# Kernel optimization log

Hardware: AMD Instinct MI355X
Metric: run time of the kernel (lower is better)

Reference implementation:

```python
import jax, jax.numpy as jnp
import numpy as np

HIDDEN = 1024
N_HEADS = 16
HEAD_DIM = HIDDEN // N_HEADS  # 64
SCALE = HEAD_DIM ** -0.5
B, QL, KVL = 2, 2048, 4096


def setup_inputs() -> dict:
    key = jax.random.key(0)
    ks = jax.random.split(key, 7)
    s = 0.02
    return {
        "query_states": jax.random.normal(ks[0], (B, QL, HIDDEN), jnp.float32),
        "key_states": jax.random.normal(ks[1], (B, KVL, HIDDEN), jnp.float32),
        "value_states": jax.random.normal(ks[2], (B, KVL, HIDDEN), jnp.float32),
        # torch nn.Linear weights: shape [out, in], applied as x @ W.T
        "Wq": jax.random.normal(ks[3], (HIDDEN, HIDDEN), jnp.float32) * s,
        "Wk": jax.random.normal(ks[4], (HIDDEN, HIDDEN), jnp.float32) * s,
        "Wv": jax.random.normal(ks[5], (HIDDEN, HIDDEN), jnp.float32) * s,
        "Wo": jax.random.normal(ks[6], (HIDDEN, HIDDEN), jnp.float32) * s,
    }


def reference(query_states, key_states, value_states, Wq, Wk, Wv, Wo):
    b, ql, _ = query_states.shape
    kvl = key_states.shape[1]
    # projections (torch Linear: x @ W.T)
    q = query_states @ Wq.T  # [b, ql, H]
    k = key_states @ Wk.T    # [b, kvl, H]
    v = value_states @ Wv.T  # [b, kvl, H]
    # split heads -> [b, h, s, d]
    q = q.reshape(b, ql, N_HEADS, HEAD_DIM).transpose(0, 2, 1, 3)
    k = k.reshape(b, kvl, N_HEADS, HEAD_DIM).transpose(0, 2, 1, 3)
    v = v.reshape(b, kvl, N_HEADS, HEAD_DIM).transpose(0, 2, 1, 3)
    # scores [b, h, ql, kvl]
    scores = jnp.einsum("bhqd,bhkd->bhqk", q, k) * SCALE
    attn = jax.nn.softmax(scores, axis=-1)
    out = jnp.einsum("bhqk,bhkd->bhqd", attn, v)  # [b, h, ql, d]
    out = out.transpose(0, 2, 1, 3).reshape(b, ql, HIDDEN)
    return out @ Wo.T
```

## Files before the change

### kernel.cpp

```cpp
#include <hip/hip_runtime.h>

#define HID   1024
#define NH    16
#define HD    64
#define QL    2048
#define KVL   4096
#define NB    2
#define QSCALE 0.180336880111120426f

typedef short s8v  __attribute__((ext_vector_type(8)));
typedef short s4v  __attribute__((ext_vector_type(4)));
typedef float f4v  __attribute__((ext_vector_type(4)));

__device__ __forceinline__ unsigned short f2bf(float f) {
  unsigned int u = __builtin_bit_cast(unsigned int, f);
  u += 0x7FFFu + ((u >> 16) & 1u);
  return (unsigned short)(u >> 16);
}
__device__ __forceinline__ float bf2f(unsigned short h) {
  unsigned int u = ((unsigned int)h) << 16;
  return __builtin_bit_cast(float, u);
}
__device__ __forceinline__ float fexp2(float x) {
#if __has_builtin(__builtin_amdgcn_exp2f)
  return __builtin_amdgcn_exp2f(x);
#else
  return exp2f(x);
#endif
}

__global__ __launch_bounds__(256)
void cast_all(const float* __restrict__ q, const float* __restrict__ k,
              const float* __restrict__ v, const float* __restrict__ wq,
              const float* __restrict__ wk, const float* __restrict__ wv,
              const float* __restrict__ wo, unsigned short* __restrict__ dst) {
  size_t c = (size_t)blockIdx.x * 256 + threadIdx.x;
  const float* src; size_t lc; float sc = 1.0f;
  if (c < 524288)       { src = q;  lc = c; }
  else if (c < 1572864) { src = k;  lc = c - 524288; }
  else if (c < 2621440) { src = v;  lc = c - 1572864; }
  else if (c < 2752512) { src = wq; lc = c - 2621440; sc = QSCALE; }
  else if (c < 2883584) { src = wk; lc = c - 2752512; }
  else if (c < 3014656) { src = wv; lc = c - 2883584; }
  else                  { src = wo; lc = c - 3014656; }
  const float4* p = (const float4*)(src + lc * 8);
  float4 a = p[0], b = p[1];
  union { s8v v8; unsigned short h[8]; } u;
  u.h[0] = f2bf(a.x * sc); u.h[1] = f2bf(a.y * sc);
  u.h[2] = f2bf(a.z * sc); u.h[3] = f2bf(a.w * sc);
  u.h[4] = f2bf(b.x * sc); u.h[5] = f2bf(b.y * sc);
  u.h[6] = f2bf(b.z * sc); u.h[7] = f2bf(b.w * sc);
  *(s8v*)(dst + c * 8) = u.v8;
}

typedef const __attribute__((address_space(1))) unsigned int* gas_t;
typedef __attribute__((address_space(3))) unsigned int*       las_t;

__device__ __forceinline__ void gl_lds16(const unsigned short* g, unsigned short* l) {
  __builtin_amdgcn_global_load_lds((gas_t)(const void*)g, (las_t)(void*)l, 16, 0, 0);
}

template <bool OUT_BF16>
__device__ __forceinline__ void gemm_body(const unsigned short* __restrict__ A,
                                          const unsigned short* __restrict__ B,
                                          void* __restrict__ Cv, int N, int K,
                                          int bx, int by,
                                          unsigned short (*As)[128 * 32],
                                          unsigned short (*Bs)[128 * 32]) {
  const int tid  = threadIdx.x;
  const int wave = tid >> 6, lane = tid & 63;
  const int wm = wave >> 1, wn = wave & 1;
  const int quad = lane >> 4, l15 = lane & 15;
  const int row0 = by * 128;
  const int col0 = bx * 128;
  const int srow = lane >> 2;
  const int scol = (lane & 3) * 8;

  f4v acc[4][4] = {};

#define G_STAGE(KI, BI)                                                         \
  {                                                                             \
    _Pragma("unroll")                                                           \
    for (int cc = 0; cc < 2; cc++) {                                            \
      int c = wave + cc * 4;                                                    \
      gl_lds16(A + (size_t)(row0 + c * 16 + srow) * K + (KI) * 32 + scol,       \
               &As[BI][c * 512]);                                               \
      gl_lds16(B + (size_t)(col0 + c * 16 + srow) * K + (KI) * 32 + scol,       \
               &Bs[BI][c * 512]);                                               \
    }                                                                           \
  }

  const int nk = K >> 5;
  G_STAGE(0, 0);
  __syncthreads();

  for (int ki = 0; ki < nk; ki++) {
    const int cur = ki & 1;
    if (ki + 1 < nk) G_STAGE(ki + 1, 1 - cur);

    s8v af[4], bf[4];
#pragma unroll
    for (int i = 0; i < 4; i++)
      af[i] = *(const s8v*)&As[cur][(wm * 64 + i * 16 + l15) * 32 + quad * 8];
#pragma unroll
    for (int j = 0; j < 4; j++)
      bf[j] = *(const s8v*)&Bs[cur][(wn * 64 + j * 16 + l15) * 32 + quad * 8];
#pragma unroll
    for (int i = 0; i < 4; i++)
#pragma unroll
      for (int j = 0; j < 4; j++)
        acc[i][j] = __builtin_amdgcn_mfma_f32_16x16x32_bf16(af[i], bf[j],
                                                            acc[i][j], 0, 0, 0);
    __syncthreads();
  }
#undef G_STAGE

#pragma unroll
  for (int i = 0; i < 4; i++) {
#pragma unroll
    for (int j = 0; j < 4; j++) {
      int r = row0 + wm * 64 + i * 16 + quad * 4;
      int c = col0 + wn * 64 + j * 16 + l15;
#pragma unroll
      for (int reg = 0; reg < 4; reg++) {
        float v = acc[i][j][reg];
        if constexpr (OUT_BF16)
          ((unsigned short*)Cv)[(size_t)(r + reg) * N + c] = f2bf(v);
        else
          ((float*)Cv)[(size_t)(r + reg) * N + c] = v;
      }
    }
  }
}

__global__ __launch_bounds__(256, 4)
void proj_fused(const unsigned short* __restrict__ qc, const unsigned short* __restrict__ kc,
                const unsigned short* __restrict__ vc, const unsigned short* __restrict__ wqc,
                const unsigned short* __restrict__ wkc, const unsigned short* __restrict__ wvc,
                unsigned short* __restrict__ qp, unsigned short* __restrict__ kp,
                unsigned short* __restrict__ vpt) {
  __shared__ unsigned short As[2][128 * 32];
  __shared__ unsigned short Bs[2][128 * 32];
  int bid = blockIdx.x;
  if (bid < 256) {
    gemm_body<true>(qc, wqc, qp, HID, HID, bid & 7, bid >> 3, As, Bs);
  } else if (bid < 768) {
    int l = bid - 256;
    gemm_body<true>(kc, wkc, kp, HID, HID, l & 7, l >> 3, As, Bs);
  } else {
    int l = bid - 768;
    int b = l >> 8, r = l & 255;
    gemm_body<true>(wvc, vc + (size_t)b * KVL * HID,
                    vpt + (size_t)b * HID * KVL, KVL, HID, r & 31, r >> 5, As, Bs);
  }
}

__global__ __launch_bounds__(256, 4)
void o_gemm(const unsigned short* __restrict__ ao, const unsigned short* __restrict__ woc,
            float* __restrict__ out) {
  __shared__ unsigned short As[2][128 * 32];
  __shared__ unsigned short Bs[2][128 * 32];
  int bid = blockIdx.x;
  gemm_body<false>(ao, woc, out, HID, HID, bid & 7, bid >> 3, As, Bs);
}

#define LDSK 40

template <typename T>
__device__ __forceinline__ void stage_tile(unsigned short* dst, const T* src,
                                           int ld, int tid, float sc) {
#pragma unroll
  for (int rep = 0; rep < 2; rep++) {
    int s = rep * 256 + tid;
    int row = s >> 2;
    int cs  = (s & 3) * 8;
    const T* p = src + (size_t)row * ld + cs;
    s8v val;
    if constexpr (sizeof(T) == 4) {
      float4 f0 = *(const float4*)p;
      float4 f1 = *(const float4*)(p + 4);
      union { s8v v; unsigned short h[8]; } u;
      u.h[0] = f2bf(f0.x * sc); u.h[1] = f2bf(f0.y * sc);
      u.h[2] = f2bf(f0.z * sc); u.h[3] = f2bf(f0.w * sc);
      u.h[4] = f2bf(f1.x * sc); u.h[5] = f2bf(f1.y * sc);
      u.h[6] = f2bf(f1.z * sc); u.h[7] = f2bf(f1.w * sc);
      val = u.v;
    } else {
      val = *(const s8v*)p;
    }
    *(s8v*)&dst[row * LDSK + cs] = val;
  }
}

template <typename TA, typename TB, bool OUT_BF16>
__global__ __launch_bounds__(256)
void gemm_conv(const TA* __restrict__ A, const TB* __restrict__ B,
               void* __restrict__ Cv, int M, int N, int K, float bscale,
               long long bz, long long cz) {
  __shared__ unsigned short As[128 * LDSK];
  __shared__ unsigned short Bs[128 * LDSK];
  const TB* Bp = B + (size_t)blockIdx.z * (size_t)bz;
  const int tid  = threadIdx.x;
  const int wave = tid >> 6, lane = tid & 63;
  const int wm = wave >> 1, wn = wave & 1;
  const int quad = lane >> 4, l15 = lane & 15;
  const int row0 = blockIdx.y * 128;
  const int col0 = blockIdx.x * 128;

  f4v acc[4][4] = {};

  for (int k0 = 0; k0 < K; k0 += 32) {
    __syncthreads();
    stage_tile(As, A + (size_t)row0 * K + k0, K, tid, 1.0f);
    stage_tile(Bs, Bp + (size_t)col0 * K + k0, K, tid, bscale);
    __syncthreads();

    s8v af[4], bf[4];
#pragma unroll
    for (int i = 0; i < 4; i++)
      af[i] = *(const s8v*)&As[(wm * 64 + i * 16 + l15) * LDSK + quad * 8];
#pragma unroll
    for (int j = 0; j < 4; j++)
      bf[j] = *(const s8v*)&Bs[(wn * 64 + j * 16 + l15) * LDSK + quad * 8];
#pragma unroll
    for (int i = 0; i < 4; i++)
#pragma unroll
      for (int j = 0; j < 4; j++)
        acc[i][j] = __builtin_amdgcn_mfma_f32_16x16x32_bf16(af[i], bf[j],
                                                            acc[i][j], 0, 0, 0);
  }

  char* Cp = (char*)Cv + (size_t)blockIdx.z * (size_t)cz * (OUT_BF16 ? 2 : 4);
#pragma unroll
  for (int i = 0; i < 4; i++) {
#pragma unroll
    for (int j = 0; j < 4; j++) {
      int r = row0 + wm * 64 + i * 16 + quad * 4;
      int c = col0 + wn * 64 + j * 16 + l15;
#pragma unroll
      for (int reg = 0; reg < 4; reg++) {
        float v = acc[i][j][reg];
        if constexpr (OUT_BF16)
          ((unsigned short*)Cp)[(size_t)(r + reg) * N + c] = f2bf(v);
        else
          ((float*)Cp)[(size_t)(r + reg) * N + c] = v;
      }
    }
  }
}

template <bool SPLIT>
__global__ __launch_bounds__(256, 2)
void attn6(const unsigned short* __restrict__ qp,
           const unsigned short* __restrict__ kp,
           const unsigned short* __restrict__ vpt,
           unsigned short* __restrict__ po,
           float* __restrict__ pl,
           unsigned short* __restrict__ ao) {
  __shared__ unsigned short Ks[2][64 * 64];
  __shared__ unsigned short Vt[2][64 * 64];
  __shared__ unsigned short Pt[4][64 * 64];

  const int bid  = blockIdx.x;
  const int qb   = bid & 7;
  const int h    = (bid >> 3) & 15;
  const int b    = (bid >> 7) & 1;
  const int half = SPLIT ? (bid >> 8) : 0;
  const int tid  = threadIdx.x;
  const int wave = tid >> 6, lane = tid & 63;
  const int quad = lane >> 4, l15 = lane & 15;
  const int q0   = qb * 256 + wave * 64;
  const int kvoff = half * (KVL / 2);
  const int NT   = SPLIT ? (KVL / 128) : (KVL / 64);

  const unsigned short* kbase = kp + (size_t)b * KVL * HID + h * HD + (size_t)kvoff * HID;
  const unsigned short* vbase = vpt + (size_t)(b * NH + h) * HD * KVL + kvoff;

  int prow[2], pcol[2], pbase[2];
#pragma unroll
  for (int i = 0; i < 2; i++) {
    int p = (i * 4 + wave) * 64 + lane;
    prow[i]  = p >> 3;
    pcol[i]  = ((p & 7) ^ (prow[i] & 7)) * 8;
    pbase[i] = (i * 4 + wave) * 512;
  }

  s8v qf[4][2];
#pragma unroll
  for (int nt = 0; nt < 4; nt++) {
    const size_t qrow = (size_t)(b * QL + q0 + nt * 16 + l15) * HID + h * HD;
#pragma unroll
    for (int ks = 0; ks < 2; ks++)
      qf[nt][ks] = *(const s8v*)(qp + qrow + ks * 32 + quad * 8);
  }

  float lrun[4] = {0.f, 0.f, 0.f, 0.f};
  f4v oacc[4][4] = {};

#define STAGE_KV(KT, BI)                                                        \
  {                                                                             \
    const unsigned short* kb = kbase + (size_t)((KT) * 64) * HID;               \
    const unsigned short* vb = vbase + (KT) * 64;                               \
    _Pragma("unroll")                                                           \
    for (int i = 0; i < 2; i++) {                                               \
      gl_lds16(kb + (size_t)prow[i] * HID + pcol[i], &Ks[BI][pbase[i]]);        \
      gl_lds16(vb + (size_t)prow[i] * KVL + pcol[i], &Vt[BI][pbase[i]]);        \
    }                                                                           \
  }

  STAGE_KV(0, 0);
  __syncthreads();

  for (int kt = 0; kt < NT; kt++) {
    const int cur = kt & 1;
    if (kt + 1 < NT) STAGE_KV(kt + 1, 1 - cur);

    f4v sacc[4][4] = {};
#pragma unroll
    for (int ks = 0; ks < 2; ks++)
#pragma unroll
      for (int mt = 0; mt < 4; mt++) {
        int row = mt * 16 + l15;
        int xc  = ((ks * 4 + quad) ^ (row & 7)) * 8;
        s8v kf = *(const s8v*)&Ks[cur][row * 64 + xc];
#pragma unroll
        for (int nt = 0; nt < 4; nt++)
          sacc[mt][nt] = __builtin_amdgcn_mfma_f32_16x16x32_bf16(kf, qf[nt][ks],
                                                                 sacc[mt][nt], 0, 0, 0);
      }

#pragma unroll
    for (int nt = 0; nt < 4; nt++) {
      float rs = 0.f;
#pragma unroll
      for (int mt = 0; mt < 4; mt++) {
        float p0 = fexp2(sacc[mt][nt][0]);
        float p1 = fexp2(sacc[mt][nt][1]);
        float p2 = fexp2(sacc[mt][nt][2]);
        float p3 = fexp2(sacc[mt][nt][3]);
        rs += (p0 + p1) + (p2 + p3);
        union { s4v v4; unsigned short hh[4]; } pk;
        pk.hh[0] = (unsigned short)(__builtin_bit_cast(unsigned int, p0) >> 16);
        pk.hh[1] = (unsigned short)(__builtin_bit_cast(unsigned int, p1) >> 16);
        pk.hh[2] = (unsigned short)(__builtin_bit_cast(unsigned int, p2) >> 16);
        pk.hh[3] = (unsigned short)(__builtin_bit_cast(unsigned int, p3) >> 16);
        int row = nt * 16 + l15;
        int c   = mt * 2 + (quad >> 1);
        int off = ((c ^ (row & 7)) * 8) + (quad & 1) * 4;
        *(s4v*)&Pt[wave][row * 64 + off] = pk.v4;
      }
      rs += __shfl_xor(rs, 16, 64);
      rs += __shfl_xor(rs, 32, 64);
      lrun[nt] += rs;
    }

#pragma unroll
    for (int ch = 0; ch < 2; ch++) {
      s8v vf[4];
#pragma unroll
      for (int dt = 0; dt < 4; dt++) {
        int row = dt * 16 + l15;
        int xc  = ((ch * 4 + quad) ^ (row & 7)) * 8;
        vf[dt] = *(const s8v*)&Vt[cur][row * 64 + xc];
      }
#pragma unroll
      for (int qt = 0; qt < 4; qt++) {
        int row = qt * 16 + l15;
        int xc  = ((ch * 4 + quad) ^ (row & 7)) * 8;
        s8v pf = *(const s8v*)&Pt[wave][row * 64 + xc];
#pragma unroll
        for (int dt = 0; dt < 4; dt++)
          oacc[qt][dt] = __builtin_amdgcn_mfma_f32_16x16x32_bf16(pf, vf[dt],
                                                                 oacc[qt][dt], 0, 0, 0);
      }
    }

    __syncthreads();
  }
#undef STAGE_KV

  if constexpr (SPLIT) {
    unsigned short* pob = po + (size_t)half * NB * QL * HID;
#pragma unroll
    for (int qt = 0; qt < 4; qt++) {
#pragma unroll
      for (int dt = 0; dt < 4; dt++)
#pragma unroll
        for (int r = 0; r < 4; r++) {
          int qq = q0 + qt * 16 + quad * 4 + r;
          int cc = h * HD + dt * 16 + l15;
          pob[(size_t)(b * QL + qq) * HID + cc] = f2bf(oacc[qt][dt][r]);
        }
      if (quad == 0)
        pl[(size_t)half * NB * NH * QL + (b * NH + h) * QL + q0 + qt * 16 + l15] = lrun[qt];
    }
  } else {
#pragma unroll
    for (int qt = 0; qt < 4; qt++) {
      float li = 1.0f / lrun[qt];
      float lr[4];
#pragma unroll
      for (int r = 0; r < 4; r++)
        lr[r] = __shfl(li, (lane & 48) + quad * 4 + r, 64);
#pragma unroll
      for (int dt = 0; dt < 4; dt++)
#pragma unroll
        for (int r = 0; r < 4; r++) {
          int qq = q0 + qt * 16 + quad * 4 + r;
          int cc = h * HD + dt * 16 + l15;
          ao[(size_t)(b * QL + qq) * HID + cc] = f2bf(oacc[qt][dt][r] * lr[r]);
        }
    }
  }
}

__global__ __launch_bounds__(256)
void combine(const unsigned short* __restrict__ po, const float* __restrict__ pl,
             unsigned short* __restrict__ ao) {
  int t  = blockIdx.x * 256 + threadIdx.x;
  int r  = t >> 7;
  int c8 = t & 127;
  int b = r >> 11, q = r & 2047, h = c8 >> 3;
  size_t lidx = (size_t)(b * NH + h) * QL + q;
  float l = pl[lidx] + pl[(size_t)NB * NH * QL + lidx];
  float inv = 1.0f / l;
  size_t off = (size_t)r * HID + c8 * 8;
  s8v a = *(const s8v*)(po + off);
  s8v c = *(const s8v*)(po + (size_t)NB * QL * HID + off);
  union { s8v v8; unsigned short hh[8]; } ua, uc, uo;
  ua.v8 = a; uc.v8 = c;
#pragma unroll
  for (int e = 0; e < 8; e++)
    uo.hh[e] = f2bf((bf2f(ua.hh[e]) + bf2f(uc.hh[e])) * inv);
  *(s8v*)(ao + off) = uo.v8;
}

extern "C" void kernel_launch(void* const* d_in, const int* in_sizes, int n_in,
                              void* d_out, int out_size, void* d_ws, size_t ws_size,
                              hipStream_t stream) {
  const float* q  = (const float*)d_in[0];
  const float* k  = (const float*)d_in[1];
  const float* v  = (const float*)d_in[2];
  const float* Wq = (const float*)d_in[3];
  const float* Wk = (const float*)d_in[4];
  const float* Wv = (const float*)d_in[5];
  const float* Wo = (const float*)d_in[6];
  float* out = (float*)d_out;
  char* ws = (char*)d_ws;
  dim3 blk(256);

  const long long MB = 1024 * 1024;
  if (ws_size >= (size_t)88 * MB) {
    unsigned short* qc  = (unsigned short*)(ws);
    unsigned short* kc  = (unsigned short*)(ws + 8 * MB);
    unsigned short* vc  = (unsigned short*)(ws + 24 * MB);
    unsigned short* wqc = (unsigned short*)(ws + 40 * MB);
    unsigned short* wkc = (unsigned short*)(ws + 42 * MB);
    unsigned short* wvc = (unsigned short*)(ws + 44 * MB);
    unsigned short* woc = (unsigned short*)(ws + 46 * MB);
    unsigned short* qp  = (unsigned short*)(ws + 48 * MB);
    unsigned short* kp  = (unsigned short*)(ws + 56 * MB);
    unsigned short* vpt = (unsigned short*)(ws + 72 * MB);
    unsigned short* ao  = (unsigned short*)(ws);
    unsigned short* po  = (unsigned short*)(ws + 8 * MB);
    float*          pl  = (float*)(ws + 40 * MB);

    cast_all<<<12288, blk, 0, stream>>>(q, k, v, Wq, Wk, Wv, Wo, (unsigned short*)ws);
    proj_fused<<<1280, blk, 0, stream>>>(qc, kc, vc, wqc, wkc, wvc, qp, kp, vpt);
    attn6<true><<<512, blk, 0, stream>>>(qp, kp, vpt, po, pl, nullptr);
    combine<<<2048, blk, 0, stream>>>(po, pl, ao);
    o_gemm<<<256, blk, 0, stream>>>(ao, woc, out);
  } else {
    unsigned short* qp  = (unsigned short*)(ws);
    unsigned short* kp  = (unsigned short*)(ws + 8 * MB);
    unsigned short* vpt = (unsigned short*)(ws + 24 * MB);
    unsigned short* ao  = (unsigned short*)(ws + 40 * MB);

    gemm_conv<float, float, true><<<dim3(8, 32), blk, 0, stream>>>(q, Wq, qp, NB * QL, HID, HID, QSCALE, 0, 0);
    gemm_conv<float, float, true><<<dim3(8, 64), blk, 0, stream>>>(k, Wk, kp, NB * KVL, HID, HID, 1.0f, 0, 0);
    gemm_conv<float, float, true><<<dim3(32, 8, 2), blk, 0, stream>>>(Wv, v, vpt, HID, KVL, HID, 1.0f,
                                                                      (long long)KVL * HID, (long long)HID * KVL);
    attn6<false><<<256, blk, 0, stream>>>(qp, kp, vpt, nullptr, nullptr, ao);
    gemm_conv<unsigned short, float, false><<<dim3(8, 32), blk, 0, stream>>>(ao, Wo, out, NB * QL, HID, HID, 1.0f, 0, 0);
  }
}
```

Baseline: 309.8 us.

## Switch attention to 32x32 MFMA and keep P in registers via lane swaps

The attention kernel moves from 16x16x32 to 32x32x16 bf16 MFMA tiles. The softmax probabilities are now repacked into the A-operand layout with cross-lane shuffles instead of a round-trip through shared memory, so the per-wave Pt LDS buffer is removed. It also raises wave priority around the MFMA sections. The aim is to cut LDS traffic and instruction count per tile, at the cost of extra shuffles and more accumulator registers. P is now rounded to bf16 instead of truncated.

```diff
diff --git a/kernel.cpp b/kernel.cpp
--- a/kernel.cpp
+++ b/kernel.cpp
@@ -11,6 +11,7 @@
 typedef short s8v  __attribute__((ext_vector_type(8)));
 typedef short s4v  __attribute__((ext_vector_type(4)));
 typedef float f4v  __attribute__((ext_vector_type(4)));
+typedef float f16x __attribute__((ext_vector_type(16)));
 
 __device__ __forceinline__ unsigned short f2bf(float f) {
   unsigned int u = __builtin_bit_cast(unsigned int, f);
@@ -27,6 +28,19 @@
 #else
   return exp2f(x);
 #endif
+}
+
+__device__ __forceinline__ unsigned packbf(float lo, float hi) {
+  return (unsigned)f2bf(lo) | ((unsigned)f2bf(hi) << 16);
+}
+
+__device__ __forceinline__ void plswap(unsigned &x, unsigned &y) {
+  unsigned sx = (unsigned)__shfl_xor((int)x, 32, 64);
+  unsigned sy = (unsigned)__shfl_xor((int)y, 32, 64);
+  unsigned nx = (threadIdx.x & 32) ? sy : x;
+  unsigned ny = (threadIdx.x & 32) ? y : sx;
+  x = nx;
+  y = ny;
 }
 
 __global__ __launch_bounds__(256)
@@ -251,7 +265,7 @@
 
 template <bool SPLIT>
 __global__ __launch_bounds__(256, 2)
-void attn6(const unsigned short* __restrict__ qp,
+void attn8(const unsigned short* __restrict__ qp,
            const unsigned short* __restrict__ kp,
            const unsigned short* __restrict__ vpt,
            unsigned short* __restrict__ po,
@@ -259,7 +273,6 @@
            unsigned short* __restrict__ ao) {
   __shared__ unsigned short Ks[2][64 * 64];
   __shared__ unsigned short Vt[2][64 * 64];
-  __shared__ unsigned short Pt[4][64 * 64];
 
   const int bid  = blockIdx.x;
   const int qb   = bid & 7;
@@ -268,7 +281,7 @@
   const int half = SPLIT ? (bid >> 8) : 0;
   const int tid  = threadIdx.x;
   const int wave = tid >> 6, lane = tid & 63;
-  const int quad = lane >> 4, l15 = lane & 15;
+  const int l31  = lane & 31, hi = lane >> 5;
   const int q0   = qb * 256 + wave * 64;
   const int kvoff = half * (KVL / 2);
   const int NT   = SPLIT ? (KVL / 128) : (KVL / 64);
@@ -285,17 +298,17 @@
     pbase[i] = (i * 4 + wave) * 512;
   }
 
-  s8v qf[4][2];
-#pragma unroll
-  for (int nt = 0; nt < 4; nt++) {
-    const size_t qrow = (size_t)(b * QL + q0 + nt * 16 + l15) * HID + h * HD;
-#pragma unroll
-    for (int ks = 0; ks < 2; ks++)
-      qf[nt][ks] = *(const s8v*)(qp + qrow + ks * 32 + quad * 8);
-  }
-
-  float lrun[4] = {0.f, 0.f, 0.f, 0.f};
-  f4v oacc[4][4] = {};
+  s8v qf[2][4];
+#pragma unroll
+  for (int nt = 0; nt < 2; nt++) {
+    const unsigned short* qrow = qp + (size_t)(b * QL + q0 + nt * 32 + l31) * HID + h * HD;
+#pragma unroll
+    for (int ks = 0; ks < 4; ks++)
+      qf[nt][ks] = *(const s8v*)(qrow + ks * 16 + hi * 8);
+  }
+
+  float lrun[2] = {0.f, 0.f};
+  f16x oacc[2][2] = {};
 
 #define STAGE_KV(KT, BI)                                                        \
   {                                                                             \
@@ -315,65 +328,69 @@
     const int cur = kt & 1;
     if (kt + 1 < NT) STAGE_KV(kt + 1, 1 - cur);
 
-    f4v sacc[4][4] = {};
-#pragma unroll
-    for (int ks = 0; ks < 2; ks++)
-#pragma unroll
-      for (int mt = 0; mt < 4; mt++) {
-        int row = mt * 16 + l15;
-        int xc  = ((ks * 4 + quad) ^ (row & 7)) * 8;
+    f16x sacc[2][2] = {};
+    __builtin_amdgcn_s_setprio(1);
+#pragma unroll
+    for (int ks = 0; ks < 4; ks++)
+#pragma unroll
+      for (int mt = 0; mt < 2; mt++) {
+        int row = mt * 32 + l31;
+        int xc  = ((ks * 2 + hi) ^ (row & 7)) * 8;
         s8v kf = *(const s8v*)&Ks[cur][row * 64 + xc];
 #pragma unroll
-        for (int nt = 0; nt < 4; nt++)
-          sacc[mt][nt] = __builtin_amdgcn_mfma_f32_16x16x32_bf16(kf, qf[nt][ks],
+        for (int nt = 0; nt < 2; nt++)
+          sacc[mt][nt] = __builtin_amdgcn_mfma_f32_32x32x16_bf16(kf, qf[nt][ks],
                                                                  sacc[mt][nt], 0, 0, 0);
       }
-
-#pragma unroll
-    for (int nt = 0; nt < 4; nt++) {
+    __builtin_amdgcn_s_setprio(0);
+
+    s8v paf[2][4];
+#pragma unroll
+    for (int nt = 0; nt < 2; nt++) {
       float rs = 0.f;
 #pragma unroll
-      for (int mt = 0; mt < 4; mt++) {
-        float p0 = fexp2(sacc[mt][nt][0]);
-        float p1 = fexp2(sacc[mt][nt][1]);
-        float p2 = fexp2(sacc[mt][nt][2]);
-        float p3 = fexp2(sacc[mt][nt][3]);
-        rs += (p0 + p1) + (p2 + p3);
-        union { s4v v4; unsigned short hh[4]; } pk;
-        pk.hh[0] = (unsigned short)(__builtin_bit_cast(unsigned int, p0) >> 16);
-        pk.hh[1] = (unsigned short)(__builtin_bit_cast(unsigned int, p1) >> 16);
-        pk.hh[2] = (unsigned short)(__builtin_bit_cast(unsigned int, p2) >> 16);
-        pk.hh[3] = (unsigned short)(__builtin_bit_cast(unsigned int, p3) >> 16);
-        int row = nt * 16 + l15;
-        int c   = mt * 2 + (quad >> 1);
-        int off = ((c ^ (row & 7)) * 8) + (quad & 1) * 4;
-        *(s4v*)&Pt[wave][row * 64 + off] = pk.v4;
+      for (int mt = 0; mt < 2; mt++) {
+        float e[16];
+#pragma unroll
+        for (int r = 0; r < 16; r++) e[r] = fexp2(sacc[mt][nt][r]);
+        rs += ((((e[0] + e[1]) + (e[2] + e[3])) + ((e[4] + e[5]) + (e[6] + e[7])))
+             + (((e[8] + e[9]) + (e[10] + e[11])) + ((e[12] + e[13]) + (e[14] + e[15]))));
+        unsigned w0 = packbf(e[0],  e[1]);
+        unsigned w1 = packbf(e[2],  e[3]);
+        unsigned w2 = packbf(e[4],  e[5]);
+        unsigned w3 = packbf(e[6],  e[7]);
+        unsigned w4 = packbf(e[8],  e[9]);
+        unsigned w5 = packbf(e[10], e[11]);
+        unsigned w6 = packbf(e[12], e[13]);
+        unsigned w7 = packbf(e[14], e[15]);
+        plswap(w0, w2);
+        plswap(w1, w3);
+        plswap(w4, w6);
+        plswap(w5, w7);
+        union { unsigned w[4]; s8v v; } u0, u1;
+        u0.w[0] = w0; u0.w[1] = w1; u0.w[2] = w2; u0.w[3] = w3;
+        u1.w[0] = w4; u1.w[1] = w5; u1.w[2] = w6; u1.w[3] = w7;
+        paf[nt][2 * mt]     = u0.v;
+        paf[nt][2 * mt + 1] = u1.v;
       }
-      rs += __shfl_xor(rs, 16, 64);
       rs += __shfl_xor(rs, 32, 64);
       lrun[nt] += rs;
     }
 
-#pragma unroll
-    for (int ch = 0; ch < 2; ch++) {
-      s8v vf[4];
-#pragma unroll
-      for (int dt = 0; dt < 4; dt++) {
-        int row = dt * 16 + l15;
-        int xc  = ((ch * 4 + quad) ^ (row & 7)) * 8;
-        vf[dt] = *(const s8v*)&Vt[cur][row * 64 + xc];
+    __builtin_amdgcn_s_setprio(1);
+#pragma unroll
+    for (int ks = 0; ks < 4; ks++)
+#pragma unroll
+      for (int dt = 0; dt < 2; dt++) {
+        int row = dt * 32 + l31;
+        int xc  = ((ks * 2 + hi) ^ (row & 7)) * 8;
+        s8v vf = *(const s8v*)&Vt[cur][row * 64 + xc];
+#pragma unroll
+        for (int nt = 0; nt < 2; nt++)
+          oacc[nt][dt] = __builtin_amdgcn_mfma_f32_32x32x16_bf16(paf[nt][ks], vf,
+                                                                 oacc[nt][dt], 0, 0, 0);
       }
-#pragma unroll
-      for (int qt = 0; qt < 4; qt++) {
-        int row = qt * 16 + l15;
-        int xc  = ((ch * 4 + quad) ^ (row & 7)) * 8;
-        s8v pf = *(const s8v*)&Pt[wave][row * 64 + xc];
-#pragma unroll
-        for (int dt = 0; dt < 4; dt++)
-          oacc[qt][dt] = __builtin_amdgcn_mfma_f32_16x16x32_bf16(pf, vf[dt],
-                                                                 oacc[qt][dt], 0, 0, 0);
-      }
-    }
+    __builtin_amdgcn_s_setprio(0);
 
     __syncthreads();
   }
@@ -382,33 +399,31 @@
   if constexpr (SPLIT) {
     unsigned short* pob = po + (size_t)half * NB * QL * HID;
 #pragma unroll
-    for (int qt = 0; qt < 4; qt++) {
-#pragma unroll
-      for (int dt = 0; dt < 4; dt++)
-#pragma unroll
-        for (int r = 0; r < 4; r++) {
-          int qq = q0 + qt * 16 + quad * 4 + r;
-          int cc = h * HD + dt * 16 + l15;
-          pob[(size_t)(b * QL + qq) * HID + cc] = f2bf(oacc[qt][dt][r]);
+    for (int nt = 0; nt < 2; nt++) {
+#pragma unroll
+      for (int dt = 0; dt < 2; dt++)
+#pragma unroll
+        for (int r = 0; r < 16; r++) {
+          int qq = q0 + nt * 32 + (r & 3) + 8 * (r >> 2) + 4 * hi;
+          int cc = h * HD + dt * 32 + l31;
+          pob[(size_t)(b * QL + qq) * HID + cc] = f2bf(oacc[nt][dt][r]);
         }
-      if (quad == 0)
-        pl[(size_t)half * NB * NH * QL + (b * NH + h) * QL + q0 + qt * 16 + l15] = lrun[qt];
+      if (hi == 0)
+        pl[(size_t)half * NB * NH * QL + (b * NH + h) * QL + q0 + nt * 32 + l31] = lrun[nt];
     }
   } else {
 #pragma unroll
-    for (int qt = 0; qt < 4; qt++) {
-      float li = 1.0f / lrun[qt];
-      float lr[4];
-#pragma unroll
-      for (int r = 0; r < 4; r++)
-        lr[r] = __shfl(li, (lane & 48) + quad * 4 + r, 64);
-#pragma unroll
-      for (int dt = 0; dt < 4; dt++)
-#pragma unroll
-        for (int r = 0; r < 4; r++) {
-          int qq = q0 + qt * 16 + quad * 4 + r;
-          int cc = h * HD + dt * 16 + l15;
-          ao[(size_t)(b * QL + qq) * HID + cc] = f2bf(oacc[qt][dt][r] * lr[r]);
+    for (int nt = 0; nt < 2; nt++) {
+      float li = 1.0f / lrun[nt];
+#pragma unroll
+      for (int dt = 0; dt < 2; dt++)
+#pragma unroll
+        for (int r = 0; r < 16; r++) {
+          int rr = (r & 3) + 8 * (r >> 2) + 4 * hi;
+          float lv = __shfl(li, rr, 64);
+          int qq = q0 + nt * 32 + rr;
+          int cc = h * HD + dt * 32 + l31;
+          ao[(size_t)(b * QL + qq) * HID + cc] = f2bf(oacc[nt][dt][r] * lv);
         }
     }
   }
@@ -467,7 +482,7 @@
 
     cast_all<<<12288, blk, 0, stream>>>(q, k, v, Wq, Wk, Wv, Wo, (unsigned short*)ws);
     proj_fused<<<1280, blk, 0, stream>>>(qc, kc, vc, wqc, wkc, wvc, qp, kp, vpt);
-    attn6<true><<<512, blk, 0, stream>>>(qp, kp, vpt, po, pl, nullptr);
+    attn8<true><<<512, blk, 0, stream>>>(qp, kp, vpt, po, pl, nullptr);
     combine<<<2048, blk, 0, stream>>>(po, pl, ao);
     o_gemm<<<256, blk, 0, stream>>>(ao, woc, out);
   } else {
@@ -480,7 +495,7 @@
     gemm_conv<float, float, true><<<dim3(8, 64), blk, 0, stream>>>(k, Wk, kp, NB * KVL, HID, HID, 1.0f, 0, 0);
     gemm_conv<float, float, true><<<dim3(32, 8, 2), blk, 0, stream>>>(Wv, v, vpt, HID, KVL, HID, 1.0f,
                                                                       (long long)KVL * HID, (long long)HID * KVL);
-    attn6<false><<<256, blk, 0, stream>>>(qp, kp, vpt, nullptr, nullptr, ao);
+    attn8<false><<<256, blk, 0, stream>>>(qp, kp, vpt, nullptr, nullptr, ao);
     gemm_conv<unsigned short, float, false><<<dim3(8, 32), blk, 0, stream>>>(ao, Wo, out, NB * QL, HID, HID, 1.0f, 0, 0);
   }
 }
```

After: 324.0 us. +4.6%, slower.
